# Kernel tuning notes

Measured on AMD Instinct MI355X. Metric: run time of the kernel, lower is better.

Reference implementation:

```python
import jax, jax.numpy as jnp
import numpy as np

LAMBDA_COORD = 5.0
LAMBDA_NOOBJ = 0.5
EPS = 1e-9


def _bbox_iou(px, py, pr, gx, gy, gr):
    """IoU of the axis-aligned bounding squares of two circles (x, y, r)."""
    l1, r1, t1, b1 = px - pr, px + pr, py - pr, py + pr
    l2, r2, t2, b2 = gx - gr, gx + gr, gy - gr, gy + gr
    iw = jnp.maximum(jnp.minimum(r1, r2) - jnp.maximum(l1, l2), 0.0)
    ih = jnp.maximum(jnp.minimum(b1, b2) - jnp.maximum(t1, t2), 0.0)
    inter = iw * ih
    a1 = (r1 - l1) * (b1 - t1)
    a2 = (r2 - l2) * (b2 - t2)
    return inter / (a1 + a2 - inter + EPS)


def setup_inputs() -> dict:
    key = jax.random.key(0)
    k1, k2, k3, k4 = jax.random.split(key, 4)
    B, L, G, C = 65536, 16, 8, 8
    pred = jax.random.uniform(k1, (B, G, G, C), dtype=jnp.float32)
    label_rc = jax.random.randint(k2, (B, L, 2), 0, G, dtype=jnp.int32)
    xy = jax.random.uniform(k3, (B, L, 2), dtype=jnp.float32)
    r = jax.random.uniform(k4, (B, L, 1), dtype=jnp.float32) * 0.2 + 0.01
    label_box = jnp.concatenate([xy, r], axis=-1)
    return {"pred": pred, "label_rc": label_rc, "label_box": label_box}


def reference(pred, label_rc, label_box):
    B = pred.shape[0]
    rows = label_rc[..., 0]  # [B, L]
    cols = label_rc[..., 1]
    bidx = jnp.arange(B)[:, None]
    pb = pred[bidx, rows, cols]  # [B, L, 8] responsible cell per label

    gx, gy, gr = label_box[..., 0], label_box[..., 1], label_box[..., 2]
    iou1 = _bbox_iou(pb[..., 0], pb[..., 1], pb[..., 2], gx, gy, gr)
    iou2 = _bbox_iou(pb[..., 4], pb[..., 5], pb[..., 6], gx, gy, gr)

    swap = iou2 > iou1
    cx = jnp.where(swap, pb[..., 4], pb[..., 0])
    cy = jnp.where(swap, pb[..., 5], pb[..., 1])
    cr = jnp.where(swap, pb[..., 6], pb[..., 2])
    conf = jnp.where(swap, pb[..., 7], pb[..., 3])
    un_conf = jnp.where(swap, pb[..., 3], pb[..., 7])
    bigger = jnp.where(swap, iou2, iou1)
    smaller = jnp.where(swap, iou1, iou2)

    coord_loss = LAMBDA_COORD * jnp.sum(
        (cx - gx) ** 2 + (cy - gy) ** 2 + (cr - gr) ** 2)
    cond_loss = jnp.sum((bigger - conf) ** 2)
    cond_loss = cond_loss + LAMBDA_NOOBJ * jnp.sum((smaller - un_conf) ** 2)

    # object mask over the 8x8 grid (duplicates collapse to 1, as in original)
    obj_mask = jnp.zeros(pred.shape[:3], dtype=pred.dtype).at[bidx, rows, cols].set(1.0)
    noobj = (pred[..., 3] ** 2 + pred[..., 7] ** 2) * (1.0 - obj_mask)
    cond_loss = cond_loss + LAMBDA_NOOBJ * jnp.sum(noobj)

    return (coord_loss + cond_loss) / B
```

## Files before the change

### kernel.cpp

```cpp
#include <hip/hip_runtime.h>


static constexpr float LAMBDA_COORD = 5.0f;
static constexpr float LAMBDA_NOOBJ = 0.5f;
static constexpr float EPS_F = 1e-9f;

__device__ __forceinline__ float bbox_iou(float px, float py, float pr,
                                          float gx, float gy, float gr) {
    float l1 = px - pr, r1 = px + pr, t1 = py - pr, b1 = py + pr;
    float l2 = gx - gr, r2 = gx + gr, t2 = gy - gr, b2 = gy + gr;
    float iw = fmaxf(fminf(r1, r2) - fmaxf(l1, l2), 0.0f);
    float ih = fmaxf(fminf(b1, b2) - fmaxf(t1, t2), 0.0f);
    float inter = iw * ih;
    float a1 = (r1 - l1) * (b1 - t1);
    float a2 = (r2 - l2) * (b2 - t2);
    return inter / (a1 + a2 - inter + EPS_F);
}

#define W_BATCH 16

__global__ __launch_bounds__(256) void yolo_loss_kernel(
    const float* __restrict__ pred,
    const int*   __restrict__ label_rc,
    const float* __restrict__ label_box,
    float* __restrict__ partials,
    int B, int L)
{
    __shared__ float        sp[W_BATCH * 512];
    __shared__ unsigned int owner[W_BATCH * 64];
    __shared__ float        wsum[4];

    const int tid = threadIdx.x;
    const int b0  = blockIdx.x * W_BATCH;
    const int nb  = min(W_BATCH, B - b0);

    #pragma unroll
    for (int k = 0; k < 4; ++k)
        owner[k * 256 + tid] = 0xFFFFFFFFu;

    const float4* gp = (const float4*)(pred + (size_t)b0 * 512);
    float4*       sv = (float4*)sp;
    const int     n4 = nb * 128;

    float acc = 0.0f;
    if (nb == W_BATCH) {
        float4 v[8];
        #pragma unroll
        for (int k = 0; k < 8; ++k) v[k] = gp[k * 256 + tid];
        #pragma unroll
        for (int k = 0; k < 8; ++k) {
            acc += v[k].w * v[k].w;
            sv[k * 256 + tid] = v[k];
        }
    } else {
        for (int i = tid; i < n4; i += 256) {
            float4 v = gp[i];
            acc += v.w * v.w;
            sv[i] = v;
        }
    }
    acc *= LAMBDA_NOOBJ;
    __syncthreads();

    int   cell = -1, w = 0;
    float p3 = 0.f, p7 = 0.f;
    if (tid < nb * L) {
        w = tid / L;
        const int l = tid - w * L;
        const int b = b0 + w;

        const int2 rc = *(const int2*)(label_rc + ((size_t)b * L + l) * 2);
        cell = rc.x * 8 + rc.y;
        atomicMin(&owner[w * 64 + cell], (unsigned)tid);

        const float* lb = label_box + ((size_t)b * L + l) * 3;
        const float gx = lb[0], gy = lb[1], gr = lb[2];

        const float4* cp = (const float4*)(sp + w * 512 + cell * 8);
        const float4 c0 = cp[0];
        const float4 c1 = cp[1];
        const float p0 = c0.x, p1 = c0.y, p2 = c0.z;
        const float p4 = c1.x, p5 = c1.y, p6 = c1.z;
        p3 = c0.w; p7 = c1.w;

        float iou1 = bbox_iou(p0, p1, p2, gx, gy, gr);
        float iou2 = bbox_iou(p4, p5, p6, gx, gy, gr);
        bool  sw   = iou2 > iou1;
        float cx      = sw ? p4 : p0;
        float cy      = sw ? p5 : p1;
        float cr      = sw ? p6 : p2;
        float conf    = sw ? p7 : p3;
        float un_conf = sw ? p3 : p7;
        float bigger  = sw ? iou2 : iou1;
        float smaller = sw ? iou1 : iou2;
        float dx = cx - gx, dy = cy - gy, dr = cr - gr;
        acc += LAMBDA_COORD * (dx * dx + dy * dy + dr * dr);
        float d1 = bigger - conf;
        float d2 = smaller - un_conf;
        acc += d1 * d1 + LAMBDA_NOOBJ * (d2 * d2);
    }
    __syncthreads();

    if (cell >= 0 && owner[w * 64 + cell] == (unsigned)tid)
        acc -= LAMBDA_NOOBJ * (p3 * p3 + p7 * p7);

    #pragma unroll
    for (int off = 32; off > 0; off >>= 1)
        acc += __shfl_xor(acc, off);
    const int lane = tid & 63, wv = tid >> 6;
    if (lane == 0) wsum[wv] = acc;
    __syncthreads();
    if (tid == 0)
        partials[blockIdx.x] = wsum[0] + wsum[1] + wsum[2] + wsum[3];
}

__global__ __launch_bounds__(256) void reduce_kernel(
    const float* __restrict__ partials, float* __restrict__ out,
    int n, float invB)
{
    float s = 0.0f;
    for (int i = threadIdx.x; i < n; i += 256)
        s += partials[i];
    #pragma unroll
    for (int off = 32; off > 0; off >>= 1)
        s += __shfl_xor(s, off);

    __shared__ float wsum[4];
    const int lane = threadIdx.x & 63, w = threadIdx.x >> 6;
    if (lane == 0) wsum[w] = s;
    __syncthreads();
    if (threadIdx.x == 0)
        out[0] = (wsum[0] + wsum[1] + wsum[2] + wsum[3]) * invB;
}

extern "C" void kernel_launch(void* const* d_in, const int* in_sizes, int n_in,
                              void* d_out, int out_size, void* d_ws, size_t ws_size,
                              hipStream_t stream) {
    const float* pred      = (const float*)d_in[0];
    const int*   label_rc  = (const int*)d_in[1];
    const float* label_box = (const float*)d_in[2];
    float*       out       = (float*)d_out;
    float*       partials  = (float*)d_ws;

    const int B = in_sizes[0] / 512;
    const int L = in_sizes[1] / (B * 2);
    const float invB = 1.0f / (float)B;

    const int blocks = (B + W_BATCH - 1) / W_BATCH;
    yolo_loss_kernel<<<blocks, 256, 0, stream>>>(
        pred, label_rc, label_box, partials, B, L);

    reduce_kernel<<<1, 256, 0, stream>>>(partials, out, blocks, invB);
}
```

Before: 206.4 us.

## Replace shared-memory staging with per-wave register prefetch and shuffle gathers

Each wave now processes eight batch items in sequence. For each item it holds the 512-float grid in two float4 registers per lane and prefetches the next item's grid while computing the current one. Responsible-cell values are gathered with wave shuffles instead of LDS, and duplicate-cell ownership is resolved with a shuffle scan in place of shared atomics. This removes the 32KB LDS tile and the block-wide barriers, which should raise occupancy. In exchange it adds a serial loop per wave, 16 shuffles per item, an L-iteration duplicate check, and assumes L ≤ 64.

```diff
diff --git a/kernel.cpp b/kernel.cpp
--- a/kernel.cpp
+++ b/kernel.cpp
@@ -4,6 +4,9 @@
 static constexpr float LAMBDA_COORD = 5.0f;
 static constexpr float LAMBDA_NOOBJ = 0.5f;
 static constexpr float EPS_F = 1e-9f;
+
+#define WAVES_PER_BLOCK  4
+#define BATCHES_PER_WAVE 8
 
 __device__ __forceinline__ float bbox_iou(float px, float py, float pr,
                                           float gx, float gy, float gr) {
@@ -17,97 +20,101 @@
     return inter / (a1 + a2 - inter + EPS_F);
 }
 
-#define W_BATCH 16
-
-__global__ __launch_bounds__(256) void yolo_loss_kernel(
+__global__ __launch_bounds__(256, 4) void yolo_loss_kernel(
     const float* __restrict__ pred,
     const int*   __restrict__ label_rc,
     const float* __restrict__ label_box,
     float* __restrict__ partials,
     int B, int L)
 {
-    __shared__ float        sp[W_BATCH * 512];
-    __shared__ unsigned int owner[W_BATCH * 64];
-    __shared__ float        wsum[4];
+    const int tid  = threadIdx.x;
+    const int lane = tid & 63;
+    const int wv   = tid >> 6;
 
-    const int tid = threadIdx.x;
-    const int b0  = blockIdx.x * W_BATCH;
-    const int nb  = min(W_BATCH, B - b0);
+    const long wg      = (long)blockIdx.x * WAVES_PER_BLOCK + wv;
+    const long b_begin = wg * BATCHES_PER_WAVE;
+    long       b_end   = b_begin + BATCHES_PER_WAVE;
+    if (b_end > (long)B) b_end = (long)B;
 
-    #pragma unroll
-    for (int k = 0; k < 4; ++k)
-        owner[k * 256 + tid] = 0xFFFFFFFFu;
+    const bool has_label = (lane < L);
+    float acc = 0.0f;
 
-    const float4* gp = (const float4*)(pred + (size_t)b0 * 512);
-    float4*       sv = (float4*)sp;
-    const int     n4 = nb * 128;
+    float4 v0, v1;
+    if (b_begin < b_end) {
+        const float4* gp = (const float4*)(pred + b_begin * 512);
+        v0 = gp[lane];
+        v1 = gp[lane + 64];
+    }
 
-    float acc = 0.0f;
-    if (nb == W_BATCH) {
-        float4 v[8];
-        #pragma unroll
-        for (int k = 0; k < 8; ++k) v[k] = gp[k * 256 + tid];
-        #pragma unroll
-        for (int k = 0; k < 8; ++k) {
-            acc += v[k].w * v[k].w;
-            sv[k * 256 + tid] = v[k];
+    for (long b = b_begin; b < b_end; ++b) {
+        const float4 c0 = v0, c1 = v1;
+        if (b + 1 < b_end) {
+            const float4* gp = (const float4*)(pred + (b + 1) * 512);
+            v0 = gp[lane];
+            v1 = gp[lane + 64];
         }
-    } else {
-        for (int i = tid; i < n4; i += 256) {
-            float4 v = gp[i];
-            acc += v.w * v.w;
-            sv[i] = v;
+
+        int   cell = 0;
+        float gx = 0.f, gy = 0.f, gr = 0.f;
+        if (has_label) {
+            const int2 rc = *(const int2*)(label_rc + ((size_t)b * L + lane) * 2);
+            cell = rc.x * 8 + rc.y;
+            const float* lb = label_box + ((size_t)b * L + lane) * 3;
+            gx = lb[0]; gy = lb[1]; gr = lb[2];
+        }
+
+        acc += LAMBDA_NOOBJ * (c0.w * c0.w + c1.w * c1.w);
+
+        const int  q  = cell * 2;
+        const bool lo = (q < 64);
+        const int  sA = q & 63;
+        const int  sB = sA + 1;
+
+        float p0, p1, p2, p3, p4, p5, p6, p7;
+        {
+            float a, bb;
+            a = __shfl(c0.x, sA); bb = __shfl(c1.x, sA); p0 = lo ? a : bb;
+            a = __shfl(c0.y, sA); bb = __shfl(c1.y, sA); p1 = lo ? a : bb;
+            a = __shfl(c0.z, sA); bb = __shfl(c1.z, sA); p2 = lo ? a : bb;
+            a = __shfl(c0.w, sA); bb = __shfl(c1.w, sA); p3 = lo ? a : bb;
+            a = __shfl(c0.x, sB); bb = __shfl(c1.x, sB); p4 = lo ? a : bb;
+            a = __shfl(c0.y, sB); bb = __shfl(c1.y, sB); p5 = lo ? a : bb;
+            a = __shfl(c0.z, sB); bb = __shfl(c1.z, sB); p6 = lo ? a : bb;
+            a = __shfl(c0.w, sB); bb = __shfl(c1.w, sB); p7 = lo ? a : bb;
+        }
+
+        bool owner = has_label;
+        for (int j = 0; j < L; ++j) {
+            const int cj = __shfl(cell, j);
+            if (j < lane && cj == cell) owner = false;
+        }
+
+        if (has_label) {
+            const float iou1 = bbox_iou(p0, p1, p2, gx, gy, gr);
+            const float iou2 = bbox_iou(p4, p5, p6, gx, gy, gr);
+            const bool  sw   = iou2 > iou1;
+            const float cx      = sw ? p4 : p0;
+            const float cy      = sw ? p5 : p1;
+            const float cr      = sw ? p6 : p2;
+            const float conf    = sw ? p7 : p3;
+            const float un_conf = sw ? p3 : p7;
+            const float bigger  = sw ? iou2 : iou1;
+            const float smaller = sw ? iou1 : iou2;
+            const float dx = cx - gx, dy = cy - gy, dr = cr - gr;
+            acc += LAMBDA_COORD * (dx * dx + dy * dy + dr * dr);
+            const float d1 = bigger - conf;
+            const float d2 = smaller - un_conf;
+            acc += d1 * d1 + LAMBDA_NOOBJ * (d2 * d2);
+            if (owner)
+                acc -= LAMBDA_NOOBJ * (p3 * p3 + p7 * p7);
         }
     }
-    acc *= LAMBDA_NOOBJ;
-    __syncthreads();
-
-    int   cell = -1, w = 0;
-    float p3 = 0.f, p7 = 0.f;
-    if (tid < nb * L) {
-        w = tid / L;
-        const int l = tid - w * L;
-        const int b = b0 + w;
-
-        const int2 rc = *(const int2*)(label_rc + ((size_t)b * L + l) * 2);
-        cell = rc.x * 8 + rc.y;
-        atomicMin(&owner[w * 64 + cell], (unsigned)tid);
-
-        const float* lb = label_box + ((size_t)b * L + l) * 3;
-        const float gx = lb[0], gy = lb[1], gr = lb[2];
-
-        const float4* cp = (const float4*)(sp + w * 512 + cell * 8);
-        const float4 c0 = cp[0];
-        const float4 c1 = cp[1];
-        const float p0 = c0.x, p1 = c0.y, p2 = c0.z;
-        const float p4 = c1.x, p5 = c1.y, p6 = c1.z;
-        p3 = c0.w; p7 = c1.w;
-
-        float iou1 = bbox_iou(p0, p1, p2, gx, gy, gr);
-        float iou2 = bbox_iou(p4, p5, p6, gx, gy, gr);
-        bool  sw   = iou2 > iou1;
-        float cx      = sw ? p4 : p0;
-        float cy      = sw ? p5 : p1;
-        float cr      = sw ? p6 : p2;
-        float conf    = sw ? p7 : p3;
-        float un_conf = sw ? p3 : p7;
-        float bigger  = sw ? iou2 : iou1;
-        float smaller = sw ? iou1 : iou2;
-        float dx = cx - gx, dy = cy - gy, dr = cr - gr;
-        acc += LAMBDA_COORD * (dx * dx + dy * dy + dr * dr);
-        float d1 = bigger - conf;
-        float d2 = smaller - un_conf;
-        acc += d1 * d1 + LAMBDA_NOOBJ * (d2 * d2);
-    }
-    __syncthreads();
-
-    if (cell >= 0 && owner[w * 64 + cell] == (unsigned)tid)
-        acc -= LAMBDA_NOOBJ * (p3 * p3 + p7 * p7);
 
     #pragma unroll
     for (int off = 32; off > 0; off >>= 1)
         acc += __shfl_xor(acc, off);
-    const int lane = tid & 63, wv = tid >> 6;
+
+    __shared__ float wsum[WAVES_PER_BLOCK];
     if (lane == 0) wsum[wv] = acc;
     __syncthreads();
     if (tid == 0)
@@ -146,7 +153,9 @@
     const int L = in_sizes[1] / (B * 2);
     const float invB = 1.0f / (float)B;
 
-    const int blocks = (B + W_BATCH - 1) / W_BATCH;
+    const int batches_per_block = WAVES_PER_BLOCK * BATCHES_PER_WAVE;
+    const int blocks = (B + batches_per_block - 1) / batches_per_block;
+
     yolo_loss_kernel<<<blocks, 256, 0, stream>>>(
         pred, label_rc, label_box, partials, B, L);
 
```

New measurement: 221.4 us. 7.3% more time.

## Split kernel into per-sample label blocks and nontemporal streaming noobj blocks

Applied to the files above, without the earlier changes.

Replaces the LDS-staged per-block batch with two block roles. Label blocks assign one sample per thread, gather only the 16 responsible cells straight from global memory with software-pipelined loads, and track duplicate cells with a 64-bit bitmask instead of shared-memory atomics. Separate streaming blocks compute the noobj sum of squares over all of pred with nontemporal float4 loads. This removes LDS staging and syncs, at the cost of reading the gathered cells a second time, uncoalesced per-thread gathers, and more partials for the final reduction.

```diff
diff --git a/kernel.cpp b/kernel.cpp
--- a/kernel.cpp
+++ b/kernel.cpp
@@ -4,6 +4,15 @@
 static constexpr float LAMBDA_COORD = 5.0f;
 static constexpr float LAMBDA_NOOBJ = 0.5f;
 static constexpr float EPS_F = 1e-9f;
+
+#define NSTREAM_BLOCKS 2048
+
+typedef float nfloat4 __attribute__((ext_vector_type(4)));
+
+__device__ __forceinline__ float4 nt_ld4(const float4* p) {
+    nfloat4 v = __builtin_nontemporal_load((const nfloat4*)p);
+    return make_float4(v.x, v.y, v.z, v.w);
+}
 
 __device__ __forceinline__ float bbox_iou(float px, float py, float pr,
                                           float gx, float gy, float gr) {
@@ -17,96 +26,148 @@
     return inter / (a1 + a2 - inter + EPS_F);
 }
 
-#define W_BATCH 16
+
+#define LPROC(c, pa, pb, GX, GY, GR)                                           \
+    {                                                                          \
+        const float p0 = (pa).x, p1 = (pa).y, p2 = (pa).z, p3 = (pa).w;        \
+        const float p4 = (pb).x, p5 = (pb).y, p6 = (pb).z, p7 = (pb).w;        \
+        const float iou1 = bbox_iou(p0, p1, p2, (GX), (GY), (GR));             \
+        const float iou2 = bbox_iou(p4, p5, p6, (GX), (GY), (GR));             \
+        const bool  sw_ = iou2 > iou1;                                         \
+        const float cx = sw_ ? p4 : p0;                                        \
+        const float cy = sw_ ? p5 : p1;                                        \
+        const float cr = sw_ ? p6 : p2;                                        \
+        const float conf    = sw_ ? p7 : p3;                                   \
+        const float un_conf = sw_ ? p3 : p7;                                   \
+        const float bigger  = sw_ ? iou2 : iou1;                               \
+        const float smaller = sw_ ? iou1 : iou2;                               \
+        const float dx = cx - (GX), dy = cy - (GY), dr = cr - (GR);            \
+        main_acc += LAMBDA_COORD * (dx * dx + dy * dy + dr * dr);              \
+        const float d1 = bigger - conf;                                        \
+        main_acc += d1 * d1;                                                   \
+        const float d2 = smaller - un_conf;                                    \
+        noobj_acc += d2 * d2;                                                  \
+        const unsigned long long bit_ = 1ull << (c);                           \
+        if (!(seen & bit_)) { seen |= bit_;                                    \
+            noobj_acc -= (p3 * p3 + p7 * p7); }                                \
+    }
+
+#define GIS(P, cA, cB, cC, cD, G)                                              \
+    {                                                                          \
+        P##f0 = boxp[3 * (G)];                                                 \
+        P##f1 = boxp[3 * (G) + 1];                                             \
+        P##f2 = boxp[3 * (G) + 2];                                             \
+        P##g0a = pbase[(cA) * 2]; P##g0b = pbase[(cA) * 2 + 1];                \
+        P##g1a = pbase[(cB) * 2]; P##g1b = pbase[(cB) * 2 + 1];                \
+        P##g2a = pbase[(cC) * 2]; P##g2b = pbase[(cC) * 2 + 1];                \
+        P##g3a = pbase[(cD) * 2]; P##g3b = pbase[(cD) * 2 + 1];                \
+    }
+
+#define GPROC(P, cA, cB, cC, cD)                                               \
+    {                                                                          \
+        LPROC(cA, P##g0a, P##g0b, P##f0.x, P##f0.y, P##f0.z)                   \
+        LPROC(cB, P##g1a, P##g1b, P##f0.w, P##f1.x, P##f1.y)                   \
+        LPROC(cC, P##g2a, P##g2b, P##f1.z, P##f1.w, P##f2.x)                   \
+        LPROC(cD, P##g3a, P##g3b, P##f2.y, P##f2.z, P##f2.w)                   \
+    }
 
 __global__ __launch_bounds__(256) void yolo_loss_kernel(
     const float* __restrict__ pred,
     const int*   __restrict__ label_rc,
     const float* __restrict__ label_box,
     float* __restrict__ partials,
-    int B, int L)
+    int B, int L, int nlabel)
 {
-    __shared__ float        sp[W_BATCH * 512];
-    __shared__ unsigned int owner[W_BATCH * 64];
-    __shared__ float        wsum[4];
-
     const int tid = threadIdx.x;
-    const int b0  = blockIdx.x * W_BATCH;
-    const int nb  = min(W_BATCH, B - b0);
-
-    #pragma unroll
-    for (int k = 0; k < 4; ++k)
-        owner[k * 256 + tid] = 0xFFFFFFFFu;
-
-    const float4* gp = (const float4*)(pred + (size_t)b0 * 512);
-    float4*       sv = (float4*)sp;
-    const int     n4 = nb * 128;
-
     float acc = 0.0f;
-    if (nb == W_BATCH) {
-        float4 v[8];
-        #pragma unroll
-        for (int k = 0; k < 8; ++k) v[k] = gp[k * 256 + tid];
-        #pragma unroll
-        for (int k = 0; k < 8; ++k) {
-            acc += v[k].w * v[k].w;
-            sv[k * 256 + tid] = v[k];
+
+    if ((int)blockIdx.x < nlabel) {
+        const long b = (long)blockIdx.x * 256 + tid;
+        if (b < (long)B) {
+            float main_acc = 0.0f, noobj_acc = 0.0f;
+            unsigned long long seen = 0ull;
+            const float4* pbase = (const float4*)(pred + (size_t)b * 512);
+
+            if (L == 16) {
+                const int4* rcp = (const int4*)(label_rc + (size_t)b * 32);
+                const int4 r0 = rcp[0], r1 = rcp[1], r2 = rcp[2], r3 = rcp[3];
+                const int4 r4 = rcp[4], r5 = rcp[5], r6 = rcp[6], r7 = rcp[7];
+                const int c0  = r0.x * 8 + r0.y, c1  = r0.z * 8 + r0.w;
+                const int c2  = r1.x * 8 + r1.y, c3  = r1.z * 8 + r1.w;
+                const int c4  = r2.x * 8 + r2.y, c5  = r2.z * 8 + r2.w;
+                const int c6  = r3.x * 8 + r3.y, c7  = r3.z * 8 + r3.w;
+                const int c8  = r4.x * 8 + r4.y, c9  = r4.z * 8 + r4.w;
+                const int c10 = r5.x * 8 + r5.y, c11 = r5.z * 8 + r5.w;
+                const int c12 = r6.x * 8 + r6.y, c13 = r6.z * 8 + r6.w;
+                const int c14 = r7.x * 8 + r7.y, c15 = r7.z * 8 + r7.w;
+                const float4* boxp = (const float4*)(label_box + (size_t)b * 48);
+
+                float4 Af0, Af1, Af2, Ag0a, Ag0b, Ag1a, Ag1b, Ag2a, Ag2b, Ag3a, Ag3b;
+                float4 Bf0, Bf1, Bf2, Bg0a, Bg0b, Bg1a, Bg1b, Bg2a, Bg2b, Bg3a, Bg3b;
+
+                GIS(A, c0, c1, c2, c3, 0)
+                GIS(B, c4, c5, c6, c7, 1)
+                GPROC(A, c0, c1, c2, c3)
+                GIS(A, c8, c9, c10, c11, 2)
+                GPROC(B, c4, c5, c6, c7)
+                GIS(B, c12, c13, c14, c15, 3)
+                GPROC(A, c8, c9, c10, c11)
+                GPROC(B, c12, c13, c14, c15)
+            } else {
+                for (int l = 0; l < L; ++l) {
+                    const int2 rc = *(const int2*)(label_rc + ((size_t)b * L + l) * 2);
+                    const int c = rc.x * 8 + rc.y;
+                    const float* lb = label_box + ((size_t)b * L + l) * 3;
+                    const float gx = lb[0], gy = lb[1], gr = lb[2];
+                    const float4 pa = pbase[c * 2], pb = pbase[c * 2 + 1];
+                    float GX = gx, GY = gy, GR = gr;
+                    LPROC(c, pa, pb, GX, GY, GR)
+                }
+            }
+            acc = main_acc + LAMBDA_NOOBJ * noobj_acc;
         }
     } else {
-        for (int i = tid; i < n4; i += 256) {
-            float4 v = gp[i];
-            acc += v.w * v.w;
-            sv[i] = v;
+        const long NS    = (long)NSTREAM_BLOCKS * 256;
+        const long st    = ((long)blockIdx.x - nlabel) * 256 + tid;
+        const long total = (long)B * 128;
+        const float4* gp = (const float4*)pred;
+        float nacc = 0.0f;
+
+        if (st + 15 * NS < total) {
+            const float4 v0  = nt_ld4(gp + st);
+            const float4 v1  = nt_ld4(gp + st + 1 * NS);
+            const float4 v2  = nt_ld4(gp + st + 2 * NS);
+            const float4 v3  = nt_ld4(gp + st + 3 * NS);
+            const float4 v4  = nt_ld4(gp + st + 4 * NS);
+            const float4 v5  = nt_ld4(gp + st + 5 * NS);
+            const float4 v6  = nt_ld4(gp + st + 6 * NS);
+            const float4 v7  = nt_ld4(gp + st + 7 * NS);
+            const float4 v8  = nt_ld4(gp + st + 8 * NS);
+            const float4 v9  = nt_ld4(gp + st + 9 * NS);
+            const float4 v10 = nt_ld4(gp + st + 10 * NS);
+            const float4 v11 = nt_ld4(gp + st + 11 * NS);
+            const float4 v12 = nt_ld4(gp + st + 12 * NS);
+            const float4 v13 = nt_ld4(gp + st + 13 * NS);
+            const float4 v14 = nt_ld4(gp + st + 14 * NS);
+            const float4 v15 = nt_ld4(gp + st + 15 * NS);
+            nacc = v0.w * v0.w + v1.w * v1.w + v2.w * v2.w + v3.w * v3.w
+                 + v4.w * v4.w + v5.w * v5.w + v6.w * v6.w + v7.w * v7.w
+                 + v8.w * v8.w + v9.w * v9.w + v10.w * v10.w + v11.w * v11.w
+                 + v12.w * v12.w + v13.w * v13.w + v14.w * v14.w + v15.w * v15.w;
+        } else {
+            for (long i = st; i < total; i += NS) {
+                const float4 v = nt_ld4(gp + i);
+                nacc += v.w * v.w;
+            }
         }
-    }
-    acc *= LAMBDA_NOOBJ;
-    __syncthreads();
-
-    int   cell = -1, w = 0;
-    float p3 = 0.f, p7 = 0.f;
-    if (tid < nb * L) {
-        w = tid / L;
-        const int l = tid - w * L;
-        const int b = b0 + w;
-
-        const int2 rc = *(const int2*)(label_rc + ((size_t)b * L + l) * 2);
-        cell = rc.x * 8 + rc.y;
-        atomicMin(&owner[w * 64 + cell], (unsigned)tid);
-
-        const float* lb = label_box + ((size_t)b * L + l) * 3;
-        const float gx = lb[0], gy = lb[1], gr = lb[2];
-
-        const float4* cp = (const float4*)(sp + w * 512 + cell * 8);
-        const float4 c0 = cp[0];
-        const float4 c1 = cp[1];
-        const float p0 = c0.x, p1 = c0.y, p2 = c0.z;
-        const float p4 = c1.x, p5 = c1.y, p6 = c1.z;
-        p3 = c0.w; p7 = c1.w;
-
-        float iou1 = bbox_iou(p0, p1, p2, gx, gy, gr);
-        float iou2 = bbox_iou(p4, p5, p6, gx, gy, gr);
-        bool  sw   = iou2 > iou1;
-        float cx      = sw ? p4 : p0;
-        float cy      = sw ? p5 : p1;
-        float cr      = sw ? p6 : p2;
-        float conf    = sw ? p7 : p3;
-        float un_conf = sw ? p3 : p7;
-        float bigger  = sw ? iou2 : iou1;
-        float smaller = sw ? iou1 : iou2;
-        float dx = cx - gx, dy = cy - gy, dr = cr - gr;
-        acc += LAMBDA_COORD * (dx * dx + dy * dy + dr * dr);
-        float d1 = bigger - conf;
-        float d2 = smaller - un_conf;
-        acc += d1 * d1 + LAMBDA_NOOBJ * (d2 * d2);
-    }
-    __syncthreads();
-
-    if (cell >= 0 && owner[w * 64 + cell] == (unsigned)tid)
-        acc -= LAMBDA_NOOBJ * (p3 * p3 + p7 * p7);
+        acc = LAMBDA_NOOBJ * nacc;
+    }
 
     #pragma unroll
     for (int off = 32; off > 0; off >>= 1)
         acc += __shfl_xor(acc, off);
+
+    __shared__ float wsum[4];
     const int lane = tid & 63, wv = tid >> 6;
     if (lane == 0) wsum[wv] = acc;
     __syncthreads();
@@ -146,9 +207,11 @@
     const int L = in_sizes[1] / (B * 2);
     const float invB = 1.0f / (float)B;
 
-    const int blocks = (B + W_BATCH - 1) / W_BATCH;
+    const int nlabel = (B + 255) / 256;
+    const int blocks = nlabel + NSTREAM_BLOCKS;
+
     yolo_loss_kernel<<<blocks, 256, 0, stream>>>(
-        pred, label_rc, label_box, partials, B, L);
+        pred, label_rc, label_box, partials, B, L, nlabel);
 
     reduce_kernel<<<1, 256, 0, stream>>>(partials, out, blocks, invB);
 }
```

Result: slower. 222.8 us (+7.9%).
